# Kernel tuning notes

Hardware: AMD Instinct MI355X
Metric: run time of the kernel (lower is better)

Reference implementation:

```python
import jax, jax.numpy as jnp
import numpy as np
import math

TOP_K = 2
CAP_FACTOR = 1.25
AUX_W = 0.01


def setup_inputs() -> dict:
    key = jax.random.key(0)
    k1, k2 = jax.random.split(key)
    x = jax.random.normal(k1, (8192, 4096), dtype=jnp.float32)
    # gate weight, torch init std=0.01, stored as (E, D) like nn.Linear
    gate_w = jax.random.normal(k2, (64, 4096), dtype=jnp.float32) * 0.01
    return {"x": x, "gate_w": gate_w}


def reference(x, gate_w):
    N, D = x.shape
    E = gate_w.shape[0]
    K = TOP_K
    C = max(math.ceil(CAP_FACTOR * N / E), 1)  # expert capacity

    logits = x @ gate_w.T                      # (N, E)
    probs = jax.nn.softmax(logits, axis=-1)    # (N, E)
    vals, idx = jax.lax.top_k(probs, K)        # (N, K)
    vals = vals / vals.sum(axis=-1, keepdims=True)

    # Parallel replacement of the serial double loop: flatten (N,K) row-major
    # (token-major, then k) which matches the loop iteration order exactly.
    flat_e = idx.reshape(-1)                               # (N*K,) expert ids
    oh = jax.nn.one_hot(flat_e, E, dtype=jnp.int32)        # (N*K, E)
    # exclusive prefix count of prior assignments to each expert
    pos = jnp.cumsum(oh, axis=0) - oh                      # (N*K, E)
    slot = jnp.take_along_axis(pos, flat_e[:, None], axis=1)[:, 0]  # (N*K,)
    # In the torch loop the counter saturates at C (only incremented when
    # c < C), so slot==prior_total is equivalent: kept iff prior_total < C.
    keep = slot < C
    slot_s = jnp.where(keep, slot, 0)
    tok = jnp.arange(N * K) // K

    combine_weights = jnp.zeros((N, E, C), dtype=x.dtype).at[
        tok, flat_e, slot_s].add(jnp.where(keep, vals.reshape(-1), 0.0))
    dispatch_mask = (jnp.zeros((N, E, C), dtype=jnp.int32).at[
        tok, flat_e, slot_s].add(keep.astype(jnp.int32))) > 0

    # load balancing loss
    f = oh.astype(jnp.float32).reshape(N, K, E).mean(axis=(0, 1))  # (E,)
    p = probs.mean(axis=0)                                         # (E,)
    load_loss = AUX_W * E * jnp.sum(f * p)

    return dispatch_mask, combine_weights, probs, load_loss
```

## Files before the change

### kernel.cpp

```cpp
#include <hip/hip_runtime.h>
#include <math.h>

#define N_TOK 8192
#define DIM   4096
#define NEXP  64
#define CAP   160
#define OFF_CW    (83886080ULL)
#define OFF_PROBS (167772160ULL)
#define OFF_LOSS  (168296448ULL)
#define NA    16384
#define SPLIT 8

typedef float vfloat4 __attribute__((ext_vector_type(4)));

__device__ __forceinline__ float wave_max64(float v) {
    for (int m = 1; m < 64; m <<= 1) v = fmaxf(v, __shfl_xor(v, m, 64));
    return v;
}
__device__ __forceinline__ float wave_sum64(float v) {
    for (int m = 1; m < 64; m <<= 1) v += __shfl_xor(v, m, 64);
    return v;
}
__device__ __forceinline__ void wave_argmax64(float& v, int& i) {
    for (int m = 1; m < 64; m <<= 1) {
        float ov = __shfl_xor(v, m, 64);
        int   oi = __shfl_xor(i, m, 64);
        if (ov > v || (ov == v && oi < i)) { v = ov; i = oi; }
    }
}

__global__ __launch_bounds__(256) void k_zero_gemm(const float* __restrict__ x,
                                                   const float* __restrict__ gw,
                                                   float* __restrict__ part,
                                                   float* __restrict__ out) {
    if (blockIdx.x >= 1024) {
        const int tok = blockIdx.x - 1024;
        float* dm = out + (size_t)tok * (NEXP * CAP);
        float* cw = out + OFF_CW + (size_t)tok * (NEXP * CAP);
        const vfloat4 z = {0.f, 0.f, 0.f, 0.f};
        for (int it = 0; it < 10; ++it) {
            const int o = 4 * (it * 256 + threadIdx.x);
            __builtin_nontemporal_store(z, (vfloat4*)(dm + o));
            __builtin_nontemporal_store(z, (vfloat4*)(cw + o));
        }
        return;
    }
    __shared__ float xs[64][68];
    __shared__ float wsh[64][68];
    const int tb = (blockIdx.x & 127) * 64;
    const int sy = blockIdx.x >> 7;
    const int d_begin = sy * (DIM / SPLIT);
    const int t  = threadIdx.x;
    const int tx = t & 15, ty = t >> 4;
    float acc[4][4] = {};
    for (int ci = 0; ci < (DIM / SPLIT) / 64; ++ci) {
        const int d0 = d_begin + ci * 64;
        for (int it = 0; it < 4; ++it) {
            int idx = t + 256 * it;
            int row = idx >> 4;
            int d4  = idx & 15;
            *(float4*)(&xs[row][4 * d4]) =
                *(const float4*)(x + (size_t)(tb + row) * DIM + d0 + 4 * d4);
            *(float4*)(&wsh[row][4 * d4]) =
                *(const float4*)(gw + (size_t)row * DIM + d0 + 4 * d4);
        }
        __syncthreads();
        for (int d4 = 0; d4 < 16; ++d4) {
            float4 xa[4], wb[4];
            for (int i = 0; i < 4; ++i) xa[i] = *(const float4*)(&xs[ty + 16 * i][4 * d4]);
            for (int j = 0; j < 4; ++j) wb[j] = *(const float4*)(&wsh[tx + 16 * j][4 * d4]);
            for (int i = 0; i < 4; ++i)
                for (int j = 0; j < 4; ++j) {
                    acc[i][j] = fmaf(xa[i].x, wb[j].x, acc[i][j]);
                    acc[i][j] = fmaf(xa[i].y, wb[j].y, acc[i][j]);
                    acc[i][j] = fmaf(xa[i].z, wb[j].z, acc[i][j]);
                    acc[i][j] = fmaf(xa[i].w, wb[j].w, acc[i][j]);
                }
        }
        __syncthreads();
    }
    for (int i = 0; i < 4; ++i)
        for (int j = 0; j < 4; ++j)
            part[(size_t)sy * N_TOK * NEXP +
                 (size_t)(tb + ty + 16 * i) * NEXP + (tx + 16 * j)] = acc[i][j];
}

__global__ __launch_bounds__(256) void k_router(const float* __restrict__ part,
                                                float* __restrict__ probs_out,
                                                int* __restrict__ rec_e,
                                                float* __restrict__ rec_w) {
    const int tok  = blockIdx.x * 4 + (threadIdx.x >> 6);
    const int lane = threadIdx.x & 63;
    float l = 0.f;
    for (int s = 0; s < SPLIT; ++s)
        l += part[(size_t)s * N_TOK * NEXP + (size_t)tok * NEXP + lane];
    const float m  = wave_max64(l);
    const float ex = expf(l - m);
    const float sm = wave_sum64(ex);
    const float p  = ex / sm;
    probs_out[(size_t)tok * NEXP + lane] = p;
    float v1 = p; int i1 = lane;
    wave_argmax64(v1, i1);
    float v2 = (lane == i1) ? -1.f : p; int i2 = lane;
    wave_argmax64(v2, i2);
    if (lane == 0) {
        const float denom = v1 + v2;
        rec_e[2 * tok]     = i1;
        rec_e[2 * tok + 1] = i2;
        rec_w[2 * tok]     = v1 / denom;
        rec_w[2 * tok + 1] = v2 / denom;
    }
}

__global__ __launch_bounds__(256) void k_preduce(const float* __restrict__ probs,
                                                 float* __restrict__ psum_part) {
    __shared__ float sh[256];
    const int e = threadIdx.x & 63, tg = threadIdx.x >> 6;
    const int tok0 = blockIdx.x * 128;
    float a = 0.f;
    for (int k = 0; k < 32; ++k)
        a += probs[(size_t)(tok0 + tg + 4 * k) * NEXP + e];
    sh[threadIdx.x] = a;
    __syncthreads();
    if (threadIdx.x < 64)
        psum_part[blockIdx.x * 64 + threadIdx.x] =
            sh[threadIdx.x] + sh[64 + threadIdx.x] +
            sh[128 + threadIdx.x] + sh[192 + threadIdx.x];
}

__global__ __launch_bounds__(256) void k_assign(const int* __restrict__ rec_e,
                                                int* __restrict__ rec_s,
                                                int* __restrict__ ecnt) {
    const int w    = blockIdx.x * 4 + (threadIdx.x >> 6);
    const int lane = threadIdx.x & 63;
    int base = 0;
    const unsigned long long ltmask = (1ull << lane) - 1ull;
    for (int c = 0; c < NA / 64; ++c) {
        const int i = c * 64 + lane;
        const int e = rec_e[i];
        const unsigned long long mask = __ballot(e == w);
        if (e == w) {
            const int slot = base + __popcll(mask & ltmask);
            rec_s[i] = (slot < CAP) ? slot : -1;
        }
        base += __popcll(mask);
    }
    if (lane == 0) ecnt[w] = base;
}

__global__ __launch_bounds__(256) void k_scatter(const int* __restrict__ rec_e,
                                                 const int* __restrict__ rec_s,
                                                 const float* __restrict__ rec_w,
                                                 const int* __restrict__ ecnt,
                                                 const float* __restrict__ psum_part,
                                                 float* __restrict__ out) {
    if (blockIdx.x == 64) {
        if (threadIdx.x < 64) {
            const int e = threadIdx.x;
            float ps = 0.f;
            for (int b = 0; b < 64; ++b) ps += psum_part[b * 64 + e];
            float term = ((float)ecnt[e] / (float)NA) * (ps / (float)N_TOK);
            term = wave_sum64(term);
            if (e == 0) out[OFF_LOSS] = 0.01f * 64.f * term;
        }
        return;
    }
    const int i = blockIdx.x * 256 + threadIdx.x;
    const int s = rec_s[i];
    if (s >= 0) {
        const int tok = i >> 1;
        const int e   = rec_e[i];
        const size_t off = (size_t)tok * (NEXP * CAP) + (size_t)e * CAP + s;
        out[off]          = 1.0f;
        out[OFF_CW + off] = rec_w[i];
    }
}

extern "C" void kernel_launch(void* const* d_in, const int* in_sizes, int n_in,
                              void* d_out, int out_size, void* d_ws, size_t ws_size,
                              hipStream_t stream) {
    const float* x  = (const float*)d_in[0];
    const float* gw = (const float*)d_in[1];
    float* out = (float*)d_out;

    char* w = (char*)d_ws;
    float* part      = (float*)w;
    int*   rec_e     = (int*)(w + (size_t)SPLIT * N_TOK * NEXP * 4);
    float* rec_w     = (float*)((char*)rec_e + NA * 4);
    int*   rec_s     = (int*)((char*)rec_w + NA * 4);
    float* psum_part = (float*)((char*)rec_s + NA * 4);
    int*   ecnt      = (int*)((char*)psum_part + 64 * 64 * 4);

    k_zero_gemm<<<1024 + N_TOK, 256, 0, stream>>>(x, gw, part, out);
    k_router<<<2048, 256, 0, stream>>>(part, out + OFF_PROBS, rec_e, rec_w);
    k_preduce<<<64, 256, 0, stream>>>(out + OFF_PROBS, psum_part);
    k_assign<<<16, 256, 0, stream>>>(rec_e, rec_s, ecnt);
    k_scatter<<<65, 256, 0, stream>>>(rec_e, rec_s, rec_w, ecnt, psum_part, out);
}
```

Measured before the change: 854.1 us.

## Fuse zero-fill with scatter and fold loss into assign kernel

Result: no change. 865.6 us (+1.4%).

```diff
diff --git a/kernel.cpp b/kernel.cpp
--- a/kernel.cpp
+++ b/kernel.cpp
@@ -29,22 +29,9 @@
     }
 }
 
-__global__ __launch_bounds__(256) void k_zero_gemm(const float* __restrict__ x,
-                                                   const float* __restrict__ gw,
-                                                   float* __restrict__ part,
-                                                   float* __restrict__ out) {
-    if (blockIdx.x >= 1024) {
-        const int tok = blockIdx.x - 1024;
-        float* dm = out + (size_t)tok * (NEXP * CAP);
-        float* cw = out + OFF_CW + (size_t)tok * (NEXP * CAP);
-        const vfloat4 z = {0.f, 0.f, 0.f, 0.f};
-        for (int it = 0; it < 10; ++it) {
-            const int o = 4 * (it * 256 + threadIdx.x);
-            __builtin_nontemporal_store(z, (vfloat4*)(dm + o));
-            __builtin_nontemporal_store(z, (vfloat4*)(cw + o));
-        }
-        return;
-    }
+__global__ __launch_bounds__(256) void k_gemm(const float* __restrict__ x,
+                                              const float* __restrict__ gw,
+                                              float* __restrict__ part) {
     __shared__ float xs[64][68];
     __shared__ float wsh[64][68];
     const int tb = (blockIdx.x & 127) * 64;
@@ -130,11 +117,32 @@
 
 __global__ __launch_bounds__(256) void k_assign(const int* __restrict__ rec_e,
                                                 int* __restrict__ rec_s,
-                                                int* __restrict__ ecnt) {
+                                                const float* __restrict__ psum_part,
+                                                float* __restrict__ out) {
+    if (blockIdx.x == 16) {
+        __shared__ int hcnt[64];
+        if (threadIdx.x < 64) hcnt[threadIdx.x] = 0;
+        __syncthreads();
+        for (int j = 0; j < 64; ++j) {
+            const int e = rec_e[j * 256 + threadIdx.x];
+            atomicAdd(&hcnt[e], 1);
+        }
+        __syncthreads();
+        if (threadIdx.x < 64) {
+            const int e = threadIdx.x;
+            float ps = 0.f;
+            for (int b = 0; b < 64; ++b) ps += psum_part[b * 64 + e];
+            float term = ((float)hcnt[e] / (float)NA) * (ps / (float)N_TOK);
+            term = wave_sum64(term);
+            if (e == 0) out[OFF_LOSS] = 0.01f * 64.f * term;
+        }
+        return;
+    }
     const int w    = blockIdx.x * 4 + (threadIdx.x >> 6);
     const int lane = threadIdx.x & 63;
     int base = 0;
     const unsigned long long ltmask = (1ull << lane) - 1ull;
+    #pragma unroll 4
     for (int c = 0; c < NA / 64; ++c) {
         const int i = c * 64 + lane;
         const int e = rec_e[i];
@@ -145,34 +153,35 @@
         }
         base += __popcll(mask);
     }
-    if (lane == 0) ecnt[w] = base;
-}
-
-__global__ __launch_bounds__(256) void k_scatter(const int* __restrict__ rec_e,
-                                                 const int* __restrict__ rec_s,
-                                                 const float* __restrict__ rec_w,
-                                                 const int* __restrict__ ecnt,
-                                                 const float* __restrict__ psum_part,
-                                                 float* __restrict__ out) {
-    if (blockIdx.x == 64) {
-        if (threadIdx.x < 64) {
-            const int e = threadIdx.x;
-            float ps = 0.f;
-            for (int b = 0; b < 64; ++b) ps += psum_part[b * 64 + e];
-            float term = ((float)ecnt[e] / (float)NA) * (ps / (float)N_TOK);
-            term = wave_sum64(term);
-            if (e == 0) out[OFF_LOSS] = 0.01f * 64.f * term;
-        }
-        return;
-    }
-    const int i = blockIdx.x * 256 + threadIdx.x;
-    const int s = rec_s[i];
-    if (s >= 0) {
-        const int tok = i >> 1;
-        const int e   = rec_e[i];
-        const size_t off = (size_t)tok * (NEXP * CAP) + (size_t)e * CAP + s;
-        out[off]          = 1.0f;
-        out[OFF_CW + off] = rec_w[i];
+}
+
+__global__ __launch_bounds__(256) void k_zero_scatter(const int* __restrict__ rec_e,
+                                                      const int* __restrict__ rec_s,
+                                                      const float* __restrict__ rec_w,
+                                                      float* __restrict__ out) {
+    const int t = threadIdx.x;
+    for (int tk = 0; tk < 4; ++tk) {
+        const int tok = blockIdx.x * 4 + tk;
+        const int e0 = rec_e[2 * tok],     e1 = rec_e[2 * tok + 1];
+        const int s0 = rec_s[2 * tok],     s1 = rec_s[2 * tok + 1];
+        const float w0 = rec_w[2 * tok],   w1 = rec_w[2 * tok + 1];
+        const int p0 = (s0 >= 0) ? e0 * CAP + s0 : -1;
+        const int p1 = (s1 >= 0) ? e1 * CAP + s1 : -1;
+        float* dm = out + (size_t)tok * (NEXP * CAP);
+        float* cw = out + OFF_CW + (size_t)tok * (NEXP * CAP);
+        for (int it = 0; it < 10; ++it) {
+            const int b4 = 4 * (it * 256 + t);
+            vfloat4 zd = {0.f, 0.f, 0.f, 0.f};
+            vfloat4 zc = {0.f, 0.f, 0.f, 0.f};
+            #pragma unroll
+            for (int j = 0; j < 4; ++j) {
+                const int pos = b4 + j;
+                if (pos == p0) { zd[j] = 1.0f; zc[j] = w0; }
+                if (pos == p1) { zd[j] = 1.0f; zc[j] = w1; }
+            }
+            __builtin_nontemporal_store(zd, (vfloat4*)(dm + b4));
+            __builtin_nontemporal_store(zc, (vfloat4*)(cw + b4));
+        }
     }
 }
 
@@ -189,11 +198,10 @@
     float* rec_w     = (float*)((char*)rec_e + NA * 4);
     int*   rec_s     = (int*)((char*)rec_w + NA * 4);
     float* psum_part = (float*)((char*)rec_s + NA * 4);
-    int*   ecnt      = (int*)((char*)psum_part + 64 * 64 * 4);
-
-    k_zero_gemm<<<1024 + N_TOK, 256, 0, stream>>>(x, gw, part, out);
+
+    k_gemm<<<1024, 256, 0, stream>>>(x, gw, part);
     k_router<<<2048, 256, 0, stream>>>(part, out + OFF_PROBS, rec_e, rec_w);
     k_preduce<<<64, 256, 0, stream>>>(out + OFF_PROBS, psum_part);
-    k_assign<<<16, 256, 0, stream>>>(rec_e, rec_s, ecnt);
-    k_scatter<<<65, 256, 0, stream>>>(rec_e, rec_s, rec_w, ecnt, psum_part, out);
-}
+    k_assign<<<17, 256, 0, stream>>>(rec_e, rec_s, psum_part, out);
+    k_zero_scatter<<<2048, 256, 0, stream>>>(rec_e, rec_s, rec_w, out);
+}
```
